# Kernel tuning notes

Measured on AMD Instinct MI355X. Metric: run time of the kernel, lower is better.

## Reference

```python
import jax, jax.numpy as jnp
import numpy as np

N = 50000      # nodes
E = 800000     # edges
D_IN = 128
D_H = 128
D_OUT = 64


def _glorot(key, fan_in, fan_out):
    s = float(np.sqrt(6.0 / (fan_in + fan_out)))
    return jax.random.uniform(key, (fan_in, fan_out), jnp.float32, -s, s)


def setup_inputs() -> dict:
    key = jax.random.key(0)
    ks = jax.random.split(key, 8)
    x = jax.random.normal(ks[0], (N, D_IN), jnp.float32)
    edge_index = jax.random.randint(ks[1], (2, E), 0, N, dtype=jnp.int32)
    return {
        "x": x,
        "edge_index": edge_index,
        "W0": _glorot(ks[2], D_IN, D_H), "b0": jnp.zeros((D_H,), jnp.float32),
        "W1": _glorot(ks[3], D_H, D_H),  "b1": jnp.zeros((D_H,), jnp.float32),
        "W2": _glorot(ks[4], D_H, D_H),  "b2": jnp.zeros((D_H,), jnp.float32),
        "W_out": _glorot(ks[5], D_H, D_OUT), "b_out": jnp.zeros((D_OUT,), jnp.float32),
    }


def reference(x, edge_index, W0, b0, W1, b1, W2, b2, W_out, b_out):
    src = edge_index[0]
    dst = edge_index[1]
    # GCN normalization with self-loops: deg = in-degree(dst) + 1
    deg = jax.ops.segment_sum(jnp.ones((E,), x.dtype), dst, num_segments=N) + 1.0
    dinv = jax.lax.rsqrt(deg)                       # [N]
    edge_coef = (dinv[src] * dinv[dst])[:, None]    # [E,1]
    self_coef = (dinv * dinv)[:, None]              # [N,1]

    def gcn_conv(h, W, b):
        h = h @ W                                            # [N,F]
        agg = jax.ops.segment_sum(h[src] * edge_coef, dst, num_segments=N)
        agg = agg + h * self_coef                            # self-loop term
        return agg + b

    h = x
    for W, b in ((W0, b0), (W1, b1), (W2, b2)):
        h_in = h
        h = jax.nn.relu(gcn_conv(h, W, b))  # eval mode: dropout is identity
        if h.shape == h_in.shape:
            h = h + h_in
    return h @ W_out + b_out
```

## Files before the change

kernel.cpp:

```cpp
#include <hip/hip_runtime.h>

#define N_NODES 50000
#define N_EDGES 800000
#define NB512 98

static inline int cdiv(int a, int b) { return (a + b - 1) / b; }

typedef __attribute__((ext_vector_type(8))) short s8vec;
typedef __attribute__((ext_vector_type(4))) float f32x4;

__device__ inline ushort f2b(float f) {
    uint u = __float_as_uint(f);
    uint r = (u + 0x7fffu + ((u >> 16) & 1u)) >> 16;
    return (ushort)r;
}
__device__ inline float b2f_lo(uint v) { return __uint_as_float(v << 16); }
__device__ inline float b2f_hi(uint v) { return __uint_as_float(v & 0xffff0000u); }

__device__ inline void add8(float* acc, uint4 v) {
    acc[0] += b2f_lo(v.x); acc[1] += b2f_hi(v.x);
    acc[2] += b2f_lo(v.y); acc[3] += b2f_hi(v.y);
    acc[4] += b2f_lo(v.z); acc[5] += b2f_hi(v.z);
    acc[6] += b2f_lo(v.w); acc[7] += b2f_hi(v.w);
}


__global__ __launch_bounds__(256) void k_prep(int* cnt,
                                              const float* __restrict__ W0, const float* __restrict__ W1,
                                              const float* __restrict__ W2, const float* __restrict__ Wo,
                                              ushort* Wt0, ushort* Wt1, ushort* Wt2, ushort* Wto) {
    int b = blockIdx.x;
    if (b < 196) {
        int i = b * 256 + threadIdx.x;
        if (i < N_NODES) cnt[i] = 0;
        return;
    }
    int i = (b - 196) * 256 + threadIdx.x;
    if (i < 16384) {
        int nn = i >> 7, k = i & 127;
        Wt0[i] = f2b(W0[k * 128 + nn]);
    } else if (i < 32768) {
        int j = i - 16384; int nn = j >> 7, k = j & 127;
        Wt1[j] = f2b(W1[k * 128 + nn]);
    } else if (i < 49152) {
        int j = i - 32768; int nn = j >> 7, k = j & 127;
        Wt2[j] = f2b(W2[k * 128 + nn]);
    } else if (i < 57344) {
        int j = i - 49152; int nn = j >> 7, k = j & 127;
        Wto[j] = f2b(Wo[k * 64 + nn]);
    }
}

__global__ __launch_bounds__(256) void k_count(const int* __restrict__ dst, int* cnt, int e) {
    int i = blockIdx.x * 256 + threadIdx.x;
    if (i < e) atomicAdd(&cnt[dst[i]], 1);
}


__global__ __launch_bounds__(512) void k_scan_all(const int* __restrict__ cnt,
                                                  int* rowptr, int* cursor, float* dinv,
                                                  int n, int e, int nb) {
    __shared__ int sh[512];
    int t = threadIdx.x, b = blockIdx.x;
    int start = b * 512;

    int partial = 0;
    for (int i = t; i < start; i += 512) partial += cnt[i];
    sh[t] = partial;
    __syncthreads();
    for (int off = 256; off > 0; off >>= 1) {
        if (t < off) sh[t] += sh[t + off];
        __syncthreads();
    }
    int base = sh[0];
    __syncthreads();

    int i = start + t;
    int v = (i < n) ? cnt[i] : 0;
    sh[t] = v;
    __syncthreads();
    for (int off = 1; off < 512; off <<= 1) {
        int add = (t >= off) ? sh[t - off] : 0;
        __syncthreads();
        sh[t] += add;
        __syncthreads();
    }
    if (i < n) {
        int rp = base + sh[t] - v;
        rowptr[i] = rp;
        cursor[i] = rp;
        dinv[i] = rsqrtf((float)v + 1.0f);
    }
    if (b == nb - 1 && t == 0) rowptr[n] = e;
}


template <int NCOL, bool IN_F32, bool OUT_F32, bool SCALE>
__device__ inline void mm_body(const void* __restrict__ Av, const ushort* __restrict__ Wt,
                               const float* __restrict__ bias, const float* __restrict__ dinv,
                               void* __restrict__ Cv, int n, int bid) {
    constexpr int NT = NCOL / 16;
    int wave = threadIdx.x >> 6;
    int lane = threadIdx.x & 63;
    int quad = lane >> 4;
    int lm = lane & 15;
    int row0 = bid * 128 + wave * 32;

    int rA0 = row0 + lm;      if (rA0 > n - 1) rA0 = n - 1;
    int rA1 = row0 + 16 + lm; if (rA1 > n - 1) rA1 = n - 1;

    f32x4 acc[2][NT];
#pragma unroll
    for (int r = 0; r < 2; r++)
#pragma unroll
        for (int t = 0; t < NT; t++) acc[r][t] = (f32x4){0.f, 0.f, 0.f, 0.f};

    for (int kc = 0; kc < 128; kc += 32) {
        s8vec af[2];
        if (IN_F32) {
            const float* A = (const float*)Av;
#pragma unroll
            for (int r = 0; r < 2; r++) {
                const float* p = A + (size_t)(r ? rA1 : rA0) * 128 + quad * 8 + kc;
                float4 a = *(const float4*)p, b = *(const float4*)(p + 4);
                s8vec v;
                v[0] = (short)f2b(a.x); v[1] = (short)f2b(a.y);
                v[2] = (short)f2b(a.z); v[3] = (short)f2b(a.w);
                v[4] = (short)f2b(b.x); v[5] = (short)f2b(b.y);
                v[6] = (short)f2b(b.z); v[7] = (short)f2b(b.w);
                af[r] = v;
            }
        } else {
            const ushort* A = (const ushort*)Av;
            af[0] = *(const s8vec*)(A + (size_t)rA0 * 128 + quad * 8 + kc);
            af[1] = *(const s8vec*)(A + (size_t)rA1 * 128 + quad * 8 + kc);
        }
#pragma unroll
        for (int t = 0; t < NT; t++) {
            s8vec bf = *(const s8vec*)(Wt + (size_t)(t * 16 + lm) * 128 + kc + quad * 8);
            acc[0][t] = __builtin_amdgcn_mfma_f32_16x16x32_bf16(af[0], bf, acc[0][t], 0, 0, 0);
            acc[1][t] = __builtin_amdgcn_mfma_f32_16x16x32_bf16(af[1], bf, acc[1][t], 0, 0, 0);
        }
    }

#pragma unroll
    for (int r = 0; r < 2; r++) {
#pragma unroll
        for (int i = 0; i < 4; i++) {
            int rr = row0 + r * 16 + quad * 4 + i;
            if (rr < n) {
                float dv = SCALE ? dinv[rr] : 1.0f;
#pragma unroll
                for (int t = 0; t < NT; t++) {
                    int col = t * 16 + lm;
                    if (OUT_F32)
                        ((float*)Cv)[(size_t)rr * NCOL + col] = acc[r][t][i] + bias[col];
                    else
                        ((ushort*)Cv)[(size_t)rr * 128 + col] =
                            f2b(SCALE ? acc[r][t][i] * dv : acc[r][t][i]);
                }
            }
        }
    }
}

template <int NCOL, bool IN_F32, bool OUT_F32, bool SCALE>
__global__ __launch_bounds__(256) void k_mm(const void* __restrict__ Av,
                                            const ushort* __restrict__ Wt,
                                            const float* __restrict__ bias,
                                            const float* __restrict__ dinv,
                                            void* __restrict__ Cv, int n) {
    mm_body<NCOL, IN_F32, OUT_F32, SCALE>(Av, Wt, bias, dinv, Cv, n, blockIdx.x);
}

__global__ __launch_bounds__(256) void k_mm0_fill(const void* __restrict__ Av,
                                                  const ushort* __restrict__ Wt,
                                                  const float* __restrict__ dinv,
                                                  void* __restrict__ Cv, int n, int mmblocks,
                                                  const int* __restrict__ src, const int* __restrict__ dst,
                                                  int* cursor, uint* ed, int e) {
    if ((int)blockIdx.x >= mmblocks) {
        int base = ((int)blockIdx.x - mmblocks) * 1024 + threadIdx.x;
#pragma unroll
        for (int k = 0; k < 4; k++) {
            int i = base + k * 256;
            if (i < e) {
                int d = dst[i], s = src[i];
                int pos = atomicAdd(&cursor[d], 1);
                ed[pos] = (uint)s;
            }
        }
        return;
    }
    mm_body<128, true, false, true>(Av, Wt, nullptr, dinv, Cv, n, blockIdx.x);
}


template <bool RES_F32>
__global__ __launch_bounds__(256) void k_gatherb(const uint4* __restrict__ T4,
                                                 const int* __restrict__ rowptr,
                                                 const uint* __restrict__ ed,
                                                 const float* __restrict__ dinv,
                                                 const float* __restrict__ bias,
                                                 const void* __restrict__ resv,
                                                 uint4* __restrict__ out4, int n) {
    int node = blockIdx.x * 16 + (threadIdx.x >> 4);
    if (node >= n) return;
    int ql = threadIdx.x & 15;
    int qb = threadIdx.x & 48;

    float acc[8] = {0.f, 0.f, 0.f, 0.f, 0.f, 0.f, 0.f, 0.f};
    int beg = rowptr[node], end = rowptr[node + 1];

    for (int base = beg; base < end; base += 16) {
        int m = end - base; if (m > 16) m = 16;
        int idx = base + ql; if (idx > end - 1) idx = end - 1;
        uint em = ed[idx];
        int j = 0;
        for (; j + 8 <= m; j += 8) {
            int s0 = __shfl((int)em, qb + j);
            int s1 = __shfl((int)em, qb + j + 1);
            int s2 = __shfl((int)em, qb + j + 2);
            int s3 = __shfl((int)em, qb + j + 3);
            int s4 = __shfl((int)em, qb + j + 4);
            int s5 = __shfl((int)em, qb + j + 5);
            int s6 = __shfl((int)em, qb + j + 6);
            int s7 = __shfl((int)em, qb + j + 7);
            uint4 v0 = T4[(size_t)s0 * 16 + ql];
            uint4 v1 = T4[(size_t)s1 * 16 + ql];
            uint4 v2 = T4[(size_t)s2 * 16 + ql];
            uint4 v3 = T4[(size_t)s3 * 16 + ql];
            uint4 v4 = T4[(size_t)s4 * 16 + ql];
            uint4 v5 = T4[(size_t)s5 * 16 + ql];
            uint4 v6 = T4[(size_t)s6 * 16 + ql];
            uint4 v7 = T4[(size_t)s7 * 16 + ql];
            add8(acc, v0); add8(acc, v1); add8(acc, v2); add8(acc, v3);
            add8(acc, v4); add8(acc, v5); add8(acc, v6); add8(acc, v7);
        }
        for (; j + 4 <= m; j += 4) {
            int s0 = __shfl((int)em, qb + j);
            int s1 = __shfl((int)em, qb + j + 1);
            int s2 = __shfl((int)em, qb + j + 2);
            int s3 = __shfl((int)em, qb + j + 3);
            uint4 v0 = T4[(size_t)s0 * 16 + ql];
            uint4 v1 = T4[(size_t)s1 * 16 + ql];
            uint4 v2 = T4[(size_t)s2 * 16 + ql];
            uint4 v3 = T4[(size_t)s3 * 16 + ql];
            add8(acc, v0); add8(acc, v1); add8(acc, v2); add8(acc, v3);
        }
        for (; j < m; j++) {
            int s = __shfl((int)em, qb + j);
            uint4 v = T4[(size_t)s * 16 + ql];
            add8(acc, v);
        }
    }

    uint4 vs = T4[(size_t)node * 16 + ql];
    add8(acc, vs);

    float di = dinv[node];
    float4 bv0 = ((const float4*)bias)[ql * 2];
    float4 bv1 = ((const float4*)bias)[ql * 2 + 1];
    float bb[8] = {bv0.x, bv0.y, bv0.z, bv0.w, bv1.x, bv1.y, bv1.z, bv1.w};

    float r[8];
    if (RES_F32) {
        float4 r0 = ((const float4*)resv)[(size_t)node * 32 + ql * 2];
        float4 r1 = ((const float4*)resv)[(size_t)node * 32 + ql * 2 + 1];
        r[0] = r0.x; r[1] = r0.y; r[2] = r0.z; r[3] = r0.w;
        r[4] = r1.x; r[5] = r1.y; r[6] = r1.z; r[7] = r1.w;
    } else {
        uint4 rv = ((const uint4*)resv)[(size_t)node * 16 + ql];
        r[0] = b2f_lo(rv.x); r[1] = b2f_hi(rv.x); r[2] = b2f_lo(rv.y); r[3] = b2f_hi(rv.y);
        r[4] = b2f_lo(rv.z); r[5] = b2f_hi(rv.z); r[6] = b2f_lo(rv.w); r[7] = b2f_hi(rv.w);
    }

    float o[8];
#pragma unroll
    for (int i = 0; i < 8; i++)
        o[i] = fmaxf(acc[i] * di + bb[i], 0.f) + r[i];

    uint4 ov;
    ov.x = (uint)f2b(o[0]) | ((uint)f2b(o[1]) << 16);
    ov.y = (uint)f2b(o[2]) | ((uint)f2b(o[3]) << 16);
    ov.z = (uint)f2b(o[4]) | ((uint)f2b(o[5]) << 16);
    ov.w = (uint)f2b(o[6]) | ((uint)f2b(o[7]) << 16);
    out4[(size_t)node * 16 + ql] = ov;
}


extern "C" void kernel_launch(void* const* d_in, const int* in_sizes, int n_in,
                              void* d_out, int out_size, void* d_ws, size_t ws_size,
                              hipStream_t stream) {
    const float* x  = (const float*)d_in[0];
    const int* eidx = (const int*)d_in[1];
    const float* W0 = (const float*)d_in[2];
    const float* b0 = (const float*)d_in[3];
    const float* W1 = (const float*)d_in[4];
    const float* b1 = (const float*)d_in[5];
    const float* W2 = (const float*)d_in[6];
    const float* b2 = (const float*)d_in[7];
    const float* Wo = (const float*)d_in[8];
    const float* bo = (const float*)d_in[9];
    float* out = (float*)d_out;

    const int N = N_NODES, E = N_EDGES;
    const int* srcI = eidx;
    const int* dstI = eidx + E;

    char* ws = (char*)d_ws;
    auto alloc = [&](size_t bytes) { char* p = ws; ws += (bytes + 255) / 256 * 256; return p; };
    int*    cnt    = (int*)alloc((size_t)N * 4);
    int*    cursor = (int*)alloc((size_t)N * 4);
    int*    rowptr = (int*)alloc((size_t)(N + 1) * 4);
    float*  dinv   = (float*)alloc((size_t)N * 4);
    uint*   ed     = (uint*)alloc((size_t)E * 4);
    ushort* tmpb   = (ushort*)alloc((size_t)N * 128 * 2);
    ushort* hAb    = (ushort*)alloc((size_t)N * 128 * 2);
    ushort* hBb    = (ushort*)alloc((size_t)N * 128 * 2);
    ushort* Wt0    = (ushort*)alloc(128 * 128 * 2);
    ushort* Wt1    = (ushort*)alloc(128 * 128 * 2);
    ushort* Wt2    = (ushort*)alloc(128 * 128 * 2);
    ushort* Wto    = (ushort*)alloc(64 * 128 * 2);

    dim3 b256(256), b512(512);

    const int mmGrid   = cdiv(N, 128);
    const int fillGrid = cdiv(E, 1024);
    const int gGrid    = cdiv(N, 16);

    k_prep<<<196 + 224, b256, 0, stream>>>(cnt, W0, W1, W2, Wo, Wt0, Wt1, Wt2, Wto);
    k_count<<<cdiv(E, 256), b256, 0, stream>>>(dstI, cnt, E);
    k_scan_all<<<NB512, b512, 0, stream>>>(cnt, rowptr, cursor, dinv, N, E, NB512);

    k_mm0_fill<<<mmGrid + fillGrid, b256, 0, stream>>>(x, Wt0, dinv, tmpb, N, mmGrid,
                                                       srcI, dstI, cursor, ed, E);
    k_gatherb<true><<<gGrid, b256, 0, stream>>>((const uint4*)tmpb, rowptr, ed, dinv, b0, x, (uint4*)hAb, N);

    k_mm<128, false, false, true><<<mmGrid, b256, 0, stream>>>(hAb, Wt1, nullptr, dinv, tmpb, N);
    k_gatherb<false><<<gGrid, b256, 0, stream>>>((const uint4*)tmpb, rowptr, ed, dinv, b1, hAb, (uint4*)hBb, N);

    k_mm<128, false, false, true><<<mmGrid, b256, 0, stream>>>(hBb, Wt2, nullptr, dinv, tmpb, N);
    k_gatherb<false><<<gGrid, b256, 0, stream>>>((const uint4*)tmpb, rowptr, ed, dinv, b2, hBb, (uint4*)hAb, N);

    k_mm<64, false, true, false><<<mmGrid, b256, 0, stream>>>(hAb, Wto, bo, dinv, out, N);
}
```

Measured before the change: 322.3 us.

## Fuse neighbor gather with next layer's matmul via LDS-staged MFMA

Each gather block of 16 nodes now stages its aggregated bf16 rows in shared memory and immediately runs the next layer's 128-wide matmul with MFMA, writing the dinv-scaled transformed features (or the final fp32 output). This removes three separate matmul launches and one full read of the hidden state for each of them, and the last layer no longer writes its hidden state at all. The 8-wide unrolled gather loop is dropped, which lowers register pressure but exposes less memory-level parallelism. Every block reloads W from global/L2 for a small 16-row tile, and the grid relies on N being divisible by 16 since the bounds checks were removed.

```diff
diff --git a/kernel.cpp b/kernel.cpp
--- a/kernel.cpp
+++ b/kernel.cpp
@@ -164,15 +164,6 @@
     }
 }
 
-template <int NCOL, bool IN_F32, bool OUT_F32, bool SCALE>
-__global__ __launch_bounds__(256) void k_mm(const void* __restrict__ Av,
-                                            const ushort* __restrict__ Wt,
-                                            const float* __restrict__ bias,
-                                            const float* __restrict__ dinv,
-                                            void* __restrict__ Cv, int n) {
-    mm_body<NCOL, IN_F32, OUT_F32, SCALE>(Av, Wt, bias, dinv, Cv, n, blockIdx.x);
-}
-
 __global__ __launch_bounds__(256) void k_mm0_fill(const void* __restrict__ Av,
                                                   const ushort* __restrict__ Wt,
                                                   const float* __restrict__ dinv,
@@ -196,18 +187,24 @@
 }
 
 
-template <bool RES_F32>
-__global__ __launch_bounds__(256) void k_gatherb(const uint4* __restrict__ T4,
-                                                 const int* __restrict__ rowptr,
-                                                 const uint* __restrict__ ed,
-                                                 const float* __restrict__ dinv,
-                                                 const float* __restrict__ bias,
-                                                 const void* __restrict__ resv,
-                                                 uint4* __restrict__ out4, int n) {
-    int node = blockIdx.x * 16 + (threadIdx.x >> 4);
-    if (node >= n) return;
-    int ql = threadIdx.x & 15;
-    int qb = threadIdx.x & 48;
+template <int NCOL, bool RES_F32, bool FINAL>
+__global__ __launch_bounds__(256) void k_gather_mm(const uint4* __restrict__ T4,
+                                                   const int* __restrict__ rowptr,
+                                                   const uint* __restrict__ ed,
+                                                   const float* __restrict__ dinv,
+                                                   const float* __restrict__ biasL,
+                                                   const void* __restrict__ resv,
+                                                   uint4* __restrict__ hout,
+                                                   const ushort* __restrict__ Wt,
+                                                   const float* __restrict__ bias_out,
+                                                   void* __restrict__ Cv, int n) {
+    __shared__ uint4 As4[16 * 17];
+    ushort* As = (ushort*)As4;
+
+    int tid = threadIdx.x;
+    int nl = tid >> 4, ql = tid & 15;
+    int qb = tid & 48;
+    int node = blockIdx.x * 16 + nl;
 
     float acc[8] = {0.f, 0.f, 0.f, 0.f, 0.f, 0.f, 0.f, 0.f};
     int beg = rowptr[node], end = rowptr[node + 1];
@@ -217,26 +214,6 @@
         int idx = base + ql; if (idx > end - 1) idx = end - 1;
         uint em = ed[idx];
         int j = 0;
-        for (; j + 8 <= m; j += 8) {
-            int s0 = __shfl((int)em, qb + j);
-            int s1 = __shfl((int)em, qb + j + 1);
-            int s2 = __shfl((int)em, qb + j + 2);
-            int s3 = __shfl((int)em, qb + j + 3);
-            int s4 = __shfl((int)em, qb + j + 4);
-            int s5 = __shfl((int)em, qb + j + 5);
-            int s6 = __shfl((int)em, qb + j + 6);
-            int s7 = __shfl((int)em, qb + j + 7);
-            uint4 v0 = T4[(size_t)s0 * 16 + ql];
-            uint4 v1 = T4[(size_t)s1 * 16 + ql];
-            uint4 v2 = T4[(size_t)s2 * 16 + ql];
-            uint4 v3 = T4[(size_t)s3 * 16 + ql];
-            uint4 v4 = T4[(size_t)s4 * 16 + ql];
-            uint4 v5 = T4[(size_t)s5 * 16 + ql];
-            uint4 v6 = T4[(size_t)s6 * 16 + ql];
-            uint4 v7 = T4[(size_t)s7 * 16 + ql];
-            add8(acc, v0); add8(acc, v1); add8(acc, v2); add8(acc, v3);
-            add8(acc, v4); add8(acc, v5); add8(acc, v6); add8(acc, v7);
-        }
         for (; j + 4 <= m; j += 4) {
             int s0 = __shfl((int)em, qb + j);
             int s1 = __shfl((int)em, qb + j + 1);
@@ -259,8 +236,8 @@
     add8(acc, vs);
 
     float di = dinv[node];
-    float4 bv0 = ((const float4*)bias)[ql * 2];
-    float4 bv1 = ((const float4*)bias)[ql * 2 + 1];
+    float4 bv0 = ((const float4*)biasL)[ql * 2];
+    float4 bv1 = ((const float4*)biasL)[ql * 2 + 1];
     float bb[8] = {bv0.x, bv0.y, bv0.z, bv0.w, bv1.x, bv1.y, bv1.z, bv1.w};
 
     float r[8];
@@ -285,7 +262,44 @@
     ov.y = (uint)f2b(o[2]) | ((uint)f2b(o[3]) << 16);
     ov.z = (uint)f2b(o[4]) | ((uint)f2b(o[5]) << 16);
     ov.w = (uint)f2b(o[6]) | ((uint)f2b(o[7]) << 16);
-    out4[(size_t)node * 16 + ql] = ov;
+
+    if (!FINAL) hout[(size_t)node * 16 + ql] = ov;
+    *(uint4*)&As[nl * 136 + ql * 8] = ov;
+    __syncthreads();
+
+    constexpr int NT = NCOL / 64;
+    int wave = tid >> 6;
+    int lane = tid & 63;
+    int quad = lane >> 4;
+    int lm = lane & 15;
+
+    f32x4 macc[NT];
+#pragma unroll
+    for (int t = 0; t < NT; t++) macc[t] = (f32x4){0.f, 0.f, 0.f, 0.f};
+
+    for (int kc = 0; kc < 128; kc += 32) {
+        s8vec af = *(const s8vec*)&As[lm * 136 + kc + quad * 8];
+#pragma unroll
+        for (int t = 0; t < NT; t++) {
+            int col = wave * (16 * NT) + t * 16 + lm;
+            s8vec bf = *(const s8vec*)(Wt + (size_t)col * 128 + kc + quad * 8);
+            macc[t] = __builtin_amdgcn_mfma_f32_16x16x32_bf16(af, bf, macc[t], 0, 0, 0);
+        }
+    }
+
+    int row0 = blockIdx.x * 16;
+#pragma unroll
+    for (int t = 0; t < NT; t++) {
+        int col = wave * (16 * NT) + t * 16 + lm;
+#pragma unroll
+        for (int i = 0; i < 4; i++) {
+            int rr = row0 + quad * 4 + i;
+            if (FINAL)
+                ((float*)Cv)[(size_t)rr * 64 + col] = macc[t][i] + bias_out[col];
+            else
+                ((ushort*)Cv)[(size_t)rr * 128 + col] = f2b(macc[t][i] * dinv[rr]);
+        }
+    }
 }
 
 
@@ -315,7 +329,8 @@
     int*    rowptr = (int*)alloc((size_t)(N + 1) * 4);
     float*  dinv   = (float*)alloc((size_t)N * 4);
     uint*   ed     = (uint*)alloc((size_t)E * 4);
-    ushort* tmpb   = (ushort*)alloc((size_t)N * 128 * 2);
+    ushort* tA     = (ushort*)alloc((size_t)N * 128 * 2);
+    ushort* tB     = (ushort*)alloc((size_t)N * 128 * 2);
     ushort* hAb    = (ushort*)alloc((size_t)N * 128 * 2);
     ushort* hBb    = (ushort*)alloc((size_t)N * 128 * 2);
     ushort* Wt0    = (ushort*)alloc(128 * 128 * 2);
@@ -327,21 +342,21 @@
 
     const int mmGrid   = cdiv(N, 128);
     const int fillGrid = cdiv(E, 1024);
-    const int gGrid    = cdiv(N, 16);
+    const int gGrid    = N / 16;
 
     k_prep<<<196 + 224, b256, 0, stream>>>(cnt, W0, W1, W2, Wo, Wt0, Wt1, Wt2, Wto);
     k_count<<<cdiv(E, 256), b256, 0, stream>>>(dstI, cnt, E);
     k_scan_all<<<NB512, b512, 0, stream>>>(cnt, rowptr, cursor, dinv, N, E, NB512);
 
-    k_mm0_fill<<<mmGrid + fillGrid, b256, 0, stream>>>(x, Wt0, dinv, tmpb, N, mmGrid,
+    k_mm0_fill<<<mmGrid + fillGrid, b256, 0, stream>>>(x, Wt0, dinv, tA, N, mmGrid,
                                                        srcI, dstI, cursor, ed, E);
-    k_gatherb<true><<<gGrid, b256, 0, stream>>>((const uint4*)tmpb, rowptr, ed, dinv, b0, x, (uint4*)hAb, N);
-
-    k_mm<128, false, false, true><<<mmGrid, b256, 0, stream>>>(hAb, Wt1, nullptr, dinv, tmpb, N);
-    k_gatherb<false><<<gGrid, b256, 0, stream>>>((const uint4*)tmpb, rowptr, ed, dinv, b1, hAb, (uint4*)hBb, N);
-
-    k_mm<128, false, false, true><<<mmGrid, b256, 0, stream>>>(hBb, Wt2, nullptr, dinv, tmpb, N);
-    k_gatherb<false><<<gGrid, b256, 0, stream>>>((const uint4*)tmpb, rowptr, ed, dinv, b2, hBb, (uint4*)hAb, N);
-
-    k_mm<64, false, true, false><<<mmGrid, b256, 0, stream>>>(hAb, Wto, bo, dinv, out, N);
-}
+
+    k_gather_mm<128, true, false><<<gGrid, b256, 0, stream>>>(
+        (const uint4*)tA, rowptr, ed, dinv, b0, x, (uint4*)hAb, Wt1, nullptr, tB, N);
+
+    k_gather_mm<128, false, false><<<gGrid, b256, 0, stream>>>(
+        (const uint4*)tB, rowptr, ed, dinv, b1, hAb, (uint4*)hBb, Wt2, nullptr, tA, N);
+
+    k_gather_mm<64, false, true><<<gGrid, b256, 0, stream>>>(
+        (const uint4*)tA, rowptr, ed, dinv, b2, hBb, nullptr, Wto, bo, out, N);
+}
```

New measurement: 299.8 us. 7.0% less time.
